# Kernel optimization log

Hardware: AMD Instinct MI355X
Metric: run time of the kernel (lower is better)

## Reference

```python
import jax, jax.numpy as jnp
import numpy as np

B, S, E = 2, 2048, 2048
H, KV, HD = 16, 4, 128  # num_heads, num_kv_heads, head_dim
G = H // KV             # query heads per kv head
ROPE_BASE = 10000.0


def rope_tables(dim, maxlen):
    freqs = 1.0 / ROPE_BASE ** (jnp.arange(0, dim, 2, dtype=jnp.float32) / dim)
    t = jnp.arange(maxlen, dtype=jnp.float32)
    f = jnp.outer(t, freqs)  # (maxlen, dim//2)
    return jnp.cos(f), jnp.sin(f)


def apply_rope(x, cos, sin):
    # x: (..., seq, heads, head_dim); interleaved-pair rotation
    s_len = x.shape[-3]
    c = cos[:s_len][:, None, :]
    s = sin[:s_len][:, None, :]
    x1 = x[..., ::2]
    x2 = x[..., 1::2]
    return jnp.stack([x1 * c - x2 * s, x1 * s + x2 * c], axis=-1).reshape(x.shape)


def setup_inputs() -> dict:
    key = jax.random.key(0)
    kx, kq, kk, kv, ko = jax.random.split(key, 5)
    x = jax.random.normal(kx, (B, S, E), dtype=jnp.float32)
    Wq = jax.random.normal(kq, (E, H * HD), dtype=jnp.float32) * 0.02
    Wk = jax.random.normal(kk, (E, KV * HD), dtype=jnp.float32) * 0.02
    Wv = jax.random.normal(kv, (E, KV * HD), dtype=jnp.float32) * 0.02
    Wo = jax.random.normal(ko, (H * HD, E), dtype=jnp.float32) * 0.02
    mask = jnp.tril(jnp.ones((S, S), dtype=bool))[None, None]  # causal (1,1,S,S)
    return {"x": x, "Wq": Wq, "Wk": Wk, "Wv": Wv, "Wo": Wo, "mask": mask}


def reference(x, Wq, Wk, Wv, Wo, mask):
    b, s, _ = x.shape
    cos, sin = rope_tables(HD, s)
    q = (x @ Wq).reshape(b, s, H, HD)
    k = (x @ Wk).reshape(b, s, KV, HD)
    v = (x @ Wv).reshape(b, s, KV, HD)
    q = apply_rope(q, cos, sin)
    k = apply_rope(k, cos, sin)
    if G > 1:
        k = jnp.repeat(k, G, axis=2)  # (b, s, H, HD)
        v = jnp.repeat(v, G, axis=2)
    q = jnp.transpose(q, (0, 2, 1, 3))  # (b, H, s, HD)
    k = jnp.transpose(k, (0, 2, 1, 3))
    v = jnp.transpose(v, (0, 2, 1, 3))
    scale = jnp.sqrt(jnp.float32(HD)).astype(q.dtype)
    scores = jnp.einsum("bhqd,bhkd->bhqk", q, k) / scale
    scores = jnp.where(mask, scores, jnp.finfo(scores.dtype).min)
    attn = jax.nn.softmax(scores, axis=-1)
    out = jnp.einsum("bhqk,bhkd->bhqd", attn, v)
    out = jnp.transpose(out, (0, 2, 1, 3)).reshape(b, s, H * HD)
    return out @ Wo
```

## Files before the change

kernel.cpp:

```cpp
#include <hip/hip_runtime.h>
#include <hip/hip_bf16.h>
#include <cstdint>

#define B_ 2
#define S_ 2048
#define E_ 2048
#define H_ 16
#define KV_ 4
#define HD_ 128
#define BS_ (B_*S_)
#define QKV_LD 3072
#define SM_SCALE 0.08838834764831845f
#define SC_LOG2E 0.1275424488538497f

typedef __attribute__((ext_vector_type(8))) __bf16 bf16x8;
typedef __attribute__((ext_vector_type(4))) float  floatx4;

__device__ __forceinline__ unsigned short f2bf(float f) {
  union { float f; unsigned u; } v; v.f = f;
  unsigned r = v.u + 0x7fffu + ((v.u >> 16) & 1u);
  return (unsigned short)(r >> 16);
}
__device__ __forceinline__ float bf2f(unsigned short u) {
  union { unsigned u; float f; } v; v.u = ((unsigned)u) << 16; return v.f;
}
__device__ __forceinline__ unsigned pack_bf16x2(float a, float b) {
  union { __hip_bfloat162 h; unsigned u; } v;
  v.h = __float22bfloat162_rn(make_float2(a, b));
  return v.u;
}

__device__ __forceinline__ void async_cp16(const void* g, void* l) {
  __builtin_amdgcn_global_load_lds(
      (const __attribute__((address_space(1))) void*)g,
      (__attribute__((address_space(3))) void*)l, 16, 0, 0);
}

__global__ __launch_bounds__(256)
void cvt_bf16(const float* __restrict__ src, unsigned short* __restrict__ dst,
              int n4) {
  int idx = blockIdx.x * 256 + threadIdx.x;
  if (idx >= n4) return;
  float4 v = *(const float4*)(src + (size_t)idx * 4);
  ushort4 o;
  o.x = f2bf(v.x); o.y = f2bf(v.y); o.z = f2bf(v.z); o.w = f2bf(v.w);
  *(ushort4*)(dst + (size_t)idx * 4) = o;
}

__global__ __launch_bounds__(256)
void cvt_bf16_t(const float* __restrict__ src, unsigned short* __restrict__ dst,
                int N, int dld, int noff) {
  __shared__ float tile[64 * 65];
  const int t = threadIdx.x;
  const int bk = blockIdx.y * 64, bn = blockIdx.x * 64;
  const int r = t >> 2, cg = t & 3;
#pragma unroll
  for (int i = 0; i < 4; ++i) {
    int c = cg * 16 + i * 4;
    float4 v = *(const float4*)(src + (size_t)(bk + r) * N + bn + c);
    tile[r * 65 + c] = v.x; tile[r * 65 + c + 1] = v.y;
    tile[r * 65 + c + 2] = v.z; tile[r * 65 + c + 3] = v.w;
  }
  __syncthreads();
  const int nl = t >> 2, kg = t & 3;
  union { unsigned short u[16]; uint4 q[2]; } o;
#pragma unroll
  for (int j = 0; j < 16; ++j)
    o.u[j] = f2bf(tile[(kg * 16 + j) * 65 + nl]);
  unsigned short* dp = dst + (size_t)(noff + bn + nl) * dld + bk + kg * 16;
  *(uint4*)(dp) = o.q[0];
  *(uint4*)(dp + 8) = o.q[1];
}

__global__ __launch_bounds__(256)
void rope_kernel(unsigned short* __restrict__ qkv) {
  const int PPR = 1280;
  int idx = blockIdx.x * 256 + threadIdx.x;
  if (idx >= BS_ * PPR) return;
  int row = idx / PPR, p = idx - row * PPR;
  int col = (p < 1024) ? (2 * p) : (2048 + 2 * (p - 1024));
  int d = p & 63;
  int s = row & (S_ - 1);
  float freq = expf(-(float)d * 0.14391156831212787f);
  float ang = (float)s * freq;
  float c = cosf(ang), sn = sinf(ang);
  unsigned short* ptr = qkv + (size_t)row * QKV_LD + col;
  float x1 = bf2f(ptr[0]), x2 = bf2f(ptr[1]);
  ptr[0] = f2bf(x1 * c - x2 * sn);
  ptr[1] = f2bf(x1 * sn + x2 * c);
}

__global__ __launch_bounds__(256)
void vtrans_kernel(const unsigned short* __restrict__ qkv,
                   unsigned short* __restrict__ vt) {
  __shared__ unsigned short tile[64 * 72];
  const int tid = threadIdx.x;
  const int s0 = blockIdx.x * 64;
  const int g = blockIdx.y >> 1;
  const int hh = (blockIdx.y & 1) * 64;
  const int b = g >> 2, kvh = g & 3;
#pragma unroll
  for (int i = 0; i < 2; ++i) {
    int chunk = tid + i * 256;
    int r = chunk >> 3, c = (chunk & 7) * 8;
    uint4 v = *(const uint4*)(qkv + (size_t)(b * S_ + s0 + r) * QKV_LD + 2560 + kvh * HD_ + hh + c);
    *(uint4*)(tile + r * 72 + c) = v;
  }
  __syncthreads();
#pragma unroll
  for (int i = 0; i < 2; ++i) {
    int chunk = tid + i * 256;
    int hdr = chunk >> 3, sc = (chunk & 7) * 8;
    union { unsigned short u[8]; uint4 v; } t;
#pragma unroll
    for (int j = 0; j < 8; ++j) t.u[j] = tile[(sc + j) * 72 + hdr];
    *(uint4*)(vt + (size_t)(g * HD_ + hh + hdr) * S_ + s0 + sc) = t.v;
  }
}

template<bool OUT_BF16>
__global__ __launch_bounds__(256, 2)
void gemm_tn(const unsigned short* __restrict__ A,
             const unsigned short* __restrict__ BT,
             void* __restrict__ C, int M, int N, int K) {
  __shared__ unsigned short Ash[128 * 32];
  __shared__ unsigned short Bsh[128 * 32];
  const int tid = threadIdx.x;
  const int l = tid & 63;
  const int l16 = l & 15, l4 = l >> 4;
  const int wave = tid >> 6;
  const int wm = (wave >> 1) * 64, wn = (wave & 1) * 64;
  const int bm = blockIdx.y * 128, bn = blockIdx.x * 128;

  const int srow = l >> 2;
  const int sg = (((l & 3) - (l >> 4)) & 3) * 8;

  floatx4 acc[4][4] = {};

  for (int kb = 0; kb < K; kb += 32) {
    __syncthreads();
#pragma unroll
    for (int i = 0; i < 2; ++i) {
      int cc = wave + i * 4;
      async_cp16(A + (size_t)(bm + 16 * cc + srow) * K + kb + sg, &Ash[cc * 512]);
      async_cp16(BT + (size_t)(bn + 16 * cc + srow) * K + kb + sg, &Bsh[cc * 512]);
    }
    __syncthreads();
    bf16x8 af[4], bf[4];
#pragma unroll
    for (int t = 0; t < 4; ++t) {
      int row = wm + t * 16 + l16;
      int s = (l4 + (l16 >> 2)) & 3;
      af[t] = *(const bf16x8*)(Ash + row * 32 + s * 8);
    }
#pragma unroll
    for (int t = 0; t < 4; ++t) {
      int row = wn + t * 16 + l16;
      int s = (l4 + (l16 >> 2)) & 3;
      bf[t] = *(const bf16x8*)(Bsh + row * 32 + s * 8);
    }
#pragma unroll
    for (int tm = 0; tm < 4; ++tm)
#pragma unroll
      for (int tn = 0; tn < 4; ++tn)
        acc[tm][tn] = __builtin_amdgcn_mfma_f32_16x16x32_bf16(af[tm], bf[tn], acc[tm][tn], 0, 0, 0);
  }
#pragma unroll
  for (int tm = 0; tm < 4; ++tm)
#pragma unroll
    for (int tn = 0; tn < 4; ++tn)
#pragma unroll
      for (int r = 0; r < 4; ++r) {
        int row = bm + wm + tm * 16 + l4 * 4 + r;
        int col = bn + wn + tn * 16 + l16;
        float v = acc[tm][tn][r];
        if (OUT_BF16) ((unsigned short*)C)[(size_t)row * N + col] = f2bf(v);
        else          ((float*)C)[(size_t)row * N + col] = v;
      }
}

__global__ __launch_bounds__(512, 2)
void gqa_attention(const unsigned short* __restrict__ qkv,
                   const unsigned short* __restrict__ vt,
                   unsigned short* __restrict__ out) {
  __shared__ unsigned short Ksh[2][2][32 * 128];
  __shared__ unsigned short Vsh[2][2][128 * 32];

  const int tid = threadIdx.x, l = tid & 63, wave = tid >> 6;
  const int l16 = l & 15, l4 = l >> 4;
  const int hw = wave & 3, seg = wave >> 2;
  const int g = blockIdx.x, b = g >> 2, kvh = g & 3;
  const int h = kvh * 4 + hw;
  const int y = blockIdx.y;

  const int k_subrow = l >> 4;
  const int v_subrow = l >> 2;
  const int gv = (((l & 3) - (l >> 4)) & 3) * 8;

  const unsigned short* kp[2];
  const unsigned short* vp[2];
#pragma unroll
  for (int i = 0; i < 2; ++i) {
    int cc = hw + i * 4;
    int krow = 4 * cc + k_subrow;
    int gk = (((l & 15) - krow) & 15) * 8;
    kp[i] = qkv + (size_t)(b * S_ + krow) * QKV_LD + 2048 + kvh * HD_ + gk;
    vp[i] = vt + (size_t)(g * HD_ + 16 * cc + v_subrow) * S_ + gv;
  }

  for (int phase = 0; phase < 2; ++phase) {
    const int t = phase ? (63 - y) : y;
    const int qt = t * 32;
    const int nch = t + 1;
    const int c0 = nch >> 1;
    const int st = nch - c0;

    bf16x8 qfA[4], qfB[4];
    {
      const unsigned short* qpA = qkv + (size_t)(b * S_ + qt + l16) * QKV_LD + h * HD_;
      const unsigned short* qpB = qpA + (size_t)16 * QKV_LD;
#pragma unroll
      for (int c = 0; c < 4; ++c) {
        qfA[c] = *(const bf16x8*)(qpA + c * 32 + l4 * 8);
        qfB[c] = *(const bf16x8*)(qpB + c * 32 + l4 * 8);
      }
    }
    asm volatile("s_waitcnt vmcnt(0)" ::: "memory");
    asm volatile("s_barrier" ::: "memory");

    {
      const int ci = (seg == 0) ? 0 : c0;
      const int ko = ci * 32 * QKV_LD, vo = ci * 32;
#pragma unroll
      for (int i = 0; i < 2; ++i) {
        int cc = hw + i * 4;
        async_cp16(kp[i] + ko, &Ksh[seg][0][cc * 512]);
        async_cp16(vp[i] + vo, &Vsh[seg][0][cc * 512]);
      }
    }

    float lsumA = 0.f, lsumB = 0.f;
    floatx4 accA[8] = {}, accB[8] = {};

    for (int step = 0; step < st; ++step) {
      const int cur = step & 1;
      asm volatile("s_barrier" ::: "memory");
      {
        const int cn = step + 1;
        const int cnext = (seg == 0) ? ((cn < c0) ? cn : 0)
                                     : ((cn < st) ? (c0 + cn) : 0);
        const int ko = cnext * 32 * QKV_LD, vo = cnext * 32;
#pragma unroll
        for (int i = 0; i < 2; ++i) {
          int cc = hw + i * 4;
          async_cp16(kp[i] + ko, &Ksh[seg][cur ^ 1][cc * 512]);
          async_cp16(vp[i] + vo, &Vsh[seg][cur ^ 1][cc * 512]);
        }
      }
      asm volatile("s_waitcnt vmcnt(4)\n\ts_barrier" ::: "memory");

      const bool active = (seg == 1) || (step < c0);
      if (active) {
        const bool tri = (seg == 1) && (step == st - 1);

        floatx4 sA[2] = {}, sB[2] = {};
#pragma unroll
        for (int half = 0; half < 2; ++half) {
          const int krow = half * 16 + l16;
#pragma unroll
          for (int c = 0; c < 4; ++c) {
            const int s = (c * 4 + l4 + l16) & 15;
            bf16x8 kf = *(const bf16x8*)(&Ksh[seg][cur][krow * 128 + s * 8]);
            sA[half] = __builtin_amdgcn_mfma_f32_16x16x32_bf16(kf, qfA[c], sA[half], 0, 0, 0);
            sB[half] = __builtin_amdgcn_mfma_f32_16x16x32_bf16(kf, qfB[c], sB[half], 0, 0, 0);
          }
        }

        float pA[8], pB[8];
#pragma unroll
        for (int half = 0; half < 2; ++half)
#pragma unroll
          for (int r = 0; r < 4; ++r) {
            float vA = fminf(sA[half][r] * SC_LOG2E, 80.f);
            float vB = fminf(sB[half][r] * SC_LOG2E, 80.f);
            if (tri) {
              int kk = half * 16 + l4 * 4 + r;
              if (kk > l16) vA = -3e38f;
              if (half == 1 && (l4 * 4 + r) > l16) vB = -3e38f;
            }
            float eA = exp2f(vA), eB = exp2f(vB);
            pA[half * 4 + r] = eA; lsumA += eA;
            pB[half * 4 + r] = eB; lsumB += eB;
          }

        unsigned a0 = pack_bf16x2(pA[0], pA[1]);
        unsigned a1 = pack_bf16x2(pA[2], pA[3]);
        unsigned a2 = pack_bf16x2(pA[4], pA[5]);
        unsigned a3 = pack_bf16x2(pA[6], pA[7]);
        asm("v_permlane32_swap_b32 %0, %1" : "+v"(a0), "+v"(a2));
        asm("v_permlane16_swap_b32 %0, %1" : "+v"(a0), "+v"(a2));
        asm("v_permlane32_swap_b32 %0, %1" : "+v"(a1), "+v"(a3));
        asm("v_permlane16_swap_b32 %0, %1" : "+v"(a1), "+v"(a3));
        unsigned b0 = pack_bf16x2(pB[0], pB[1]);
        unsigned b1 = pack_bf16x2(pB[2], pB[3]);
        unsigned b2 = pack_bf16x2(pB[4], pB[5]);
        unsigned b3 = pack_bf16x2(pB[6], pB[7]);
        asm("v_permlane32_swap_b32 %0, %1" : "+v"(b0), "+v"(b2));
        asm("v_permlane16_swap_b32 %0, %1" : "+v"(b0), "+v"(b2));
        asm("v_permlane32_swap_b32 %0, %1" : "+v"(b1), "+v"(b3));
        asm("v_permlane16_swap_b32 %0, %1" : "+v"(b1), "+v"(b3));
        union { unsigned w[4]; bf16x8 v8; } punA, punB;
        punA.w[0] = a0; punA.w[1] = a1; punA.w[2] = a2; punA.w[3] = a3;
        punB.w[0] = b0; punB.w[1] = b1; punB.w[2] = b2; punB.w[3] = b3;
        const bf16x8 pfA = punA.v8;
        const bf16x8 pfB = punB.v8;

#pragma unroll
        for (int u = 0; u < 8; ++u) {
          const int row = u * 16 + l16;
          const int s = (l4 + (l16 >> 2)) & 3;
          bf16x8 vf = *(const bf16x8*)(&Vsh[seg][cur][row * 32 + s * 8]);
          accA[u] = __builtin_amdgcn_mfma_f32_16x16x32_bf16(vf, pfA, accA[u], 0, 0, 0);
          accB[u] = __builtin_amdgcn_mfma_f32_16x16x32_bf16(vf, pfB, accB[u], 0, 0, 0);
        }
      }
    }

    asm volatile("s_waitcnt vmcnt(0)" ::: "memory");
    __syncthreads();
    float* combA = (float*)(&Ksh[0][0][0]);
    float* combL = (float*)(&Vsh[0][0][0]);
    if (seg == 1) {
#pragma unroll
      for (int u = 0; u < 8; ++u)
        *(floatx4*)(combA + ((hw * 8 + u) * 64 + l) * 4) = accA[u];
      combL[(hw * 64 + l) * 2]     = lsumA;
      combL[(hw * 64 + l) * 2 + 1] = lsumB;
    }
    __syncthreads();
    if (seg == 0) {
#pragma unroll
      for (int u = 0; u < 8; ++u)
        accA[u] += *(const floatx4*)(combA + ((hw * 8 + u) * 64 + l) * 4);
      lsumA += combL[(hw * 64 + l) * 2];
      lsumB += combL[(hw * 64 + l) * 2 + 1];
    }
    __syncthreads();
    if (seg == 1) {
#pragma unroll
      for (int u = 0; u < 8; ++u)
        *(floatx4*)(combA + ((hw * 8 + u) * 64 + l) * 4) = accB[u];
    }
    __syncthreads();
    if (seg == 0) {
#pragma unroll
      for (int u = 0; u < 8; ++u)
        accB[u] += *(const floatx4*)(combA + ((hw * 8 + u) * 64 + l) * 4);

      lsumA += __shfl_xor(lsumA, 16, 64);
      lsumA += __shfl_xor(lsumA, 32, 64);
      lsumB += __shfl_xor(lsumB, 16, 64);
      lsumB += __shfl_xor(lsumB, 32, 64);
      float invA = 1.0f / lsumA;
      float invB = 1.0f / lsumB;
      unsigned short* opA = out + (size_t)(b * S_ + qt + l16) * 2048 + h * HD_;
      unsigned short* opB = opA + (size_t)16 * 2048;
#pragma unroll
      for (int u = 0; u < 8; ++u) {
        uint2 oA, oB;
        oA.x = pack_bf16x2(accA[u][0] * invA, accA[u][1] * invA);
        oA.y = pack_bf16x2(accA[u][2] * invA, accA[u][3] * invA);
        *(uint2*)(opA + u * 16 + l4 * 4) = oA;
        oB.x = pack_bf16x2(accB[u][0] * invB, accB[u][1] * invB);
        oB.y = pack_bf16x2(accB[u][2] * invB, accB[u][3] * invB);
        *(uint2*)(opB + u * 16 + l4 * 4) = oB;
      }
    }
  }
}

extern "C" void kernel_launch(void* const* d_in, const int* in_sizes, int n_in,
                              void* d_out, int out_size, void* d_ws, size_t ws_size,
                              hipStream_t stream) {
  const float* x  = (const float*)d_in[0];
  const float* Wq = (const float*)d_in[1];
  const float* Wk = (const float*)d_in[2];
  const float* Wv = (const float*)d_in[3];
  const float* Wo = (const float*)d_in[4];
  float* out = (float*)d_out;

  char* ws = (char*)d_ws;
  unsigned short* xb    = (unsigned short*)(ws);
  unsigned short* wqkvT = (unsigned short*)(ws + 16777216);
  unsigned short* woT   = (unsigned short*)(ws + 29360128);
  unsigned short* qkv   = (unsigned short*)(ws + 37748736);
  unsigned short* attn  = (unsigned short*)(ws + 62914560);
  unsigned short* vt    = (unsigned short*)(ws);

  cvt_bf16<<<(4096 * 2048 / 4 + 255) / 256, 256, 0, stream>>>(x, xb, 4096 * 2048 / 4);
  cvt_bf16_t<<<dim3(32, 32), 256, 0, stream>>>(Wq, wqkvT, 2048, 2048, 0);
  cvt_bf16_t<<<dim3(8, 32),  256, 0, stream>>>(Wk, wqkvT, 512,  2048, 2048);
  cvt_bf16_t<<<dim3(8, 32),  256, 0, stream>>>(Wv, wqkvT, 512,  2048, 2560);
  cvt_bf16_t<<<dim3(32, 32), 256, 0, stream>>>(Wo, woT,  2048, 2048, 0);

  gemm_tn<true><<<dim3(24, 32), 256, 0, stream>>>(xb, wqkvT, qkv, 4096, 3072, 2048);
  rope_kernel<<<(4096 * 1280 + 255) / 256, 256, 0, stream>>>(qkv);
  vtrans_kernel<<<dim3(32, 16), 256, 0, stream>>>(qkv, vt);
  gqa_attention<<<dim3(8, 32), 512, 0, stream>>>(qkv, vt, attn);
  gemm_tn<false><<<dim3(16, 32), 256, 0, stream>>>(attn, woT, out, 4096, 2048, 2048);
}
```

Baseline: 338.0 us.

## Replace GEMM with 256x256 8-wave double-buffered pipelined kernel

Replaces the 128x128 single-buffer GEMM with a 256x256-tile, 512-thread kernel. It uses double-buffered LDS with K=64 steps, interleaves async loads with four MFMA quadrant phases, raises wave priority around MFMAs, and remaps workgroup IDs across 8 groups. The aim is to hide global load latency, halve the barrier count per unit of work and raise operand reuse in the QKV and output projections. It uses much more LDS (128KB per block) and more registers, and the grids become small (192 and 128 blocks), which may underfill the CUs.

```diff
diff --git a/kernel.cpp b/kernel.cpp
--- a/kernel.cpp
+++ b/kernel.cpp
@@ -119,64 +119,167 @@
 }
 
 template<bool OUT_BF16>
-__global__ __launch_bounds__(256, 2)
-void gemm_tn(const unsigned short* __restrict__ A,
-             const unsigned short* __restrict__ BT,
-             void* __restrict__ C, int M, int N, int K) {
-  __shared__ unsigned short Ash[128 * 32];
-  __shared__ unsigned short Bsh[128 * 32];
-  const int tid = threadIdx.x;
-  const int l = tid & 63;
+__global__ __launch_bounds__(512, 2)
+void gemm8(const unsigned short* __restrict__ A,
+           const unsigned short* __restrict__ BT,
+           void* __restrict__ C, int M, int N, int K) {
+  __shared__ unsigned short Ash[2][256 * 64];
+  __shared__ unsigned short Bsh[2][256 * 64];
+  const int tid = threadIdx.x, l = tid & 63, w = tid >> 6;
   const int l16 = l & 15, l4 = l >> 4;
-  const int wave = tid >> 6;
-  const int wm = (wave >> 1) * 64, wn = (wave & 1) * 64;
-  const int bm = blockIdx.y * 128, bn = blockIdx.x * 128;
-
-  const int srow = l >> 2;
-  const int sg = (((l & 3) - (l >> 4)) & 3) * 8;
-
-  floatx4 acc[4][4] = {};
-
-  for (int kb = 0; kb < K; kb += 32) {
-    __syncthreads();
-#pragma unroll
-    for (int i = 0; i < 2; ++i) {
-      int cc = wave + i * 4;
-      async_cp16(A + (size_t)(bm + 16 * cc + srow) * K + kb + sg, &Ash[cc * 512]);
-      async_cp16(BT + (size_t)(bn + 16 * cc + srow) * K + kb + sg, &Bsh[cc * 512]);
-    }
-    __syncthreads();
-    bf16x8 af[4], bf[4];
-#pragma unroll
-    for (int t = 0; t < 4; ++t) {
-      int row = wm + t * 16 + l16;
-      int s = (l4 + (l16 >> 2)) & 3;
-      af[t] = *(const bf16x8*)(Ash + row * 32 + s * 8);
-    }
-#pragma unroll
-    for (int t = 0; t < 4; ++t) {
-      int row = wn + t * 16 + l16;
-      int s = (l4 + (l16 >> 2)) & 3;
-      bf[t] = *(const bf16x8*)(Bsh + row * 32 + s * 8);
-    }
-#pragma unroll
-    for (int tm = 0; tm < 4; ++tm)
-#pragma unroll
-      for (int tn = 0; tn < 4; ++tn)
-        acc[tm][tn] = __builtin_amdgcn_mfma_f32_16x16x32_bf16(af[tm], bf[tn], acc[tm][tn], 0, 0, 0);
-  }
-#pragma unroll
-  for (int tm = 0; tm < 4; ++tm)
-#pragma unroll
-    for (int tn = 0; tn < 4; ++tn)
-#pragma unroll
-      for (int r = 0; r < 4; ++r) {
-        int row = bm + wm + tm * 16 + l4 * 4 + r;
-        int col = bn + wn + tn * 16 + l16;
-        float v = acc[tm][tn][r];
-        if (OUT_BF16) ((unsigned short*)C)[(size_t)row * N + col] = f2bf(v);
-        else          ((float*)C)[(size_t)row * N + col] = v;
-      }
+  const int w2 = w >> 2, w3 = w & 3;
+
+  const int ntn = (int)gridDim.x;
+  const int nwg = (int)(gridDim.x * gridDim.y);
+  const int orig = (int)blockIdx.y * ntn + (int)blockIdx.x;
+  const int cpx = nwg >> 3;
+  const int swz = (orig & 7) * cpx + (orig >> 3);
+  const int bm = (swz / ntn) * 256, bn = (swz % ntn) * 256;
+
+  const int srow = tid >> 3;
+  const int sgrp = ((tid & 7) - (tid >> 3)) & 7;
+  const unsigned short* Asrc = A  + (size_t)(bm + srow) * K + sgrp * 8;
+  const unsigned short* Bsrc = BT + (size_t)(bn + srow) * K + sgrp * 8;
+  const int ldst = w * 512;
+
+#define STAGE_A8(buf, H, kb) do { \
+    async_cp16(Asrc + (size_t)((H) * 128) * K + (kb),      &Ash[buf][(H) * 8192 + ldst]); \
+    async_cp16(Asrc + (size_t)((H) * 128 + 64) * K + (kb), &Ash[buf][(H) * 8192 + 4096 + ldst]); \
+  } while (0)
+#define STAGE_B8(buf, H, kb) do { \
+    async_cp16(Bsrc + (size_t)((H) * 128) * K + (kb),      &Bsh[buf][(H) * 8192 + ldst]); \
+    async_cp16(Bsrc + (size_t)((H) * 128 + 64) * K + (kb), &Bsh[buf][(H) * 8192 + 4096 + ldst]); \
+  } while (0)
+#define BAR8() __builtin_amdgcn_s_barrier()
+#define VMCNT4() asm volatile("s_waitcnt vmcnt(4)" ::: "memory")
+
+  const int s0 = ((l4 + l16) & 7) * 8;
+  const int s1 = ((l4 + l16 + 4) & 7) * 8;
+  const int arb = w2 * 64 + l16;
+  const int brb = w3 * 32 + l16;
+
+  const int nkt = K >> 6;
+
+  STAGE_B8(0, 0, 0);
+  STAGE_A8(0, 1, 0);
+  STAGE_A8(0, 0, 0);
+  STAGE_B8(0, 1, 0);
+  {
+    const int kb1 = (nkt > 1) ? 64 : 0;
+    STAGE_B8(1, 0, kb1);
+    STAGE_A8(1, 1, kb1);
+  }
+  VMCNT4(); BAR8();
+
+  floatx4 acc[2][4][2][2] = {};
+
+  for (int kt = 0; kt < nkt; ++kt) {
+    const int cur = kt & 1;
+    const int kb1 = ((kt + 1 < nkt) ? kt + 1 : nkt - 1) << 6;
+    const int kb2 = ((kt + 2 < nkt) ? kt + 2 : nkt - 1) << 6;
+    bf16x8 a[4][2], b0[2][2], b1[2][2];
+
+#pragma unroll
+    for (int m = 0; m < 4; ++m) {
+      const int rA = 128 + arb + m * 16;
+      a[m][0] = *(const bf16x8*)(&Ash[cur][rA * 64 + s0]);
+      a[m][1] = *(const bf16x8*)(&Ash[cur][rA * 64 + s1]);
+    }
+#pragma unroll
+    for (int n = 0; n < 2; ++n) {
+      const int rB = brb + n * 16;
+      b0[n][0] = *(const bf16x8*)(&Bsh[cur][rB * 64 + s0]);
+      b0[n][1] = *(const bf16x8*)(&Bsh[cur][rB * 64 + s1]);
+    }
+    STAGE_A8(cur ^ 1, 0, kb1);
+    BAR8();
+    __builtin_amdgcn_s_setprio(1);
+#pragma unroll
+    for (int m = 0; m < 4; ++m)
+#pragma unroll
+      for (int n = 0; n < 2; ++n) {
+        acc[1][m][0][n] = __builtin_amdgcn_mfma_f32_16x16x32_bf16(a[m][0], b0[n][0], acc[1][m][0][n], 0, 0, 0);
+        acc[1][m][0][n] = __builtin_amdgcn_mfma_f32_16x16x32_bf16(a[m][1], b0[n][1], acc[1][m][0][n], 0, 0, 0);
+      }
+    __builtin_amdgcn_s_setprio(0);
+    BAR8();
+
+#pragma unroll
+    for (int n = 0; n < 2; ++n) {
+      const int rB = 128 + brb + n * 16;
+      b1[n][0] = *(const bf16x8*)(&Bsh[cur][rB * 64 + s0]);
+      b1[n][1] = *(const bf16x8*)(&Bsh[cur][rB * 64 + s1]);
+    }
+    STAGE_B8(cur ^ 1, 1, kb1);
+    BAR8();
+    __builtin_amdgcn_s_setprio(1);
+#pragma unroll
+    for (int m = 0; m < 4; ++m)
+#pragma unroll
+      for (int n = 0; n < 2; ++n) {
+        acc[1][m][1][n] = __builtin_amdgcn_mfma_f32_16x16x32_bf16(a[m][0], b1[n][0], acc[1][m][1][n], 0, 0, 0);
+        acc[1][m][1][n] = __builtin_amdgcn_mfma_f32_16x16x32_bf16(a[m][1], b1[n][1], acc[1][m][1][n], 0, 0, 0);
+      }
+    __builtin_amdgcn_s_setprio(0);
+    BAR8();
+
+#pragma unroll
+    for (int m = 0; m < 4; ++m) {
+      const int rA = arb + m * 16;
+      a[m][0] = *(const bf16x8*)(&Ash[cur][rA * 64 + s0]);
+      a[m][1] = *(const bf16x8*)(&Ash[cur][rA * 64 + s1]);
+    }
+    STAGE_B8(cur, 0, kb2);
+    BAR8();
+    __builtin_amdgcn_s_setprio(1);
+#pragma unroll
+    for (int m = 0; m < 4; ++m)
+#pragma unroll
+      for (int n = 0; n < 2; ++n) {
+        acc[0][m][1][n] = __builtin_amdgcn_mfma_f32_16x16x32_bf16(a[m][0], b1[n][0], acc[0][m][1][n], 0, 0, 0);
+        acc[0][m][1][n] = __builtin_amdgcn_mfma_f32_16x16x32_bf16(a[m][1], b1[n][1], acc[0][m][1][n], 0, 0, 0);
+      }
+    __builtin_amdgcn_s_setprio(0);
+    BAR8();
+
+    STAGE_A8(cur, 1, kb2);
+    BAR8();
+    __builtin_amdgcn_s_setprio(1);
+#pragma unroll
+    for (int m = 0; m < 4; ++m)
+#pragma unroll
+      for (int n = 0; n < 2; ++n) {
+        acc[0][m][0][n] = __builtin_amdgcn_mfma_f32_16x16x32_bf16(a[m][0], b0[n][0], acc[0][m][0][n], 0, 0, 0);
+        acc[0][m][0][n] = __builtin_amdgcn_mfma_f32_16x16x32_bf16(a[m][1], b0[n][1], acc[0][m][0][n], 0, 0, 0);
+      }
+    __builtin_amdgcn_s_setprio(0);
+    VMCNT4();
+    BAR8();
+  }
+
+  asm volatile("s_waitcnt vmcnt(0)" ::: "memory");
+
+#pragma unroll
+  for (int mh = 0; mh < 2; ++mh)
+#pragma unroll
+    for (int m = 0; m < 4; ++m)
+#pragma unroll
+      for (int nh = 0; nh < 2; ++nh)
+#pragma unroll
+        for (int n = 0; n < 2; ++n) {
+          const int row0 = bm + mh * 128 + w2 * 64 + m * 16 + l4 * 4;
+          const int col  = bn + nh * 128 + w3 * 32 + n * 16 + l16;
+#pragma unroll
+          for (int rr = 0; rr < 4; ++rr) {
+            float v = acc[mh][m][nh][n][rr];
+            if (OUT_BF16) ((unsigned short*)C)[(size_t)(row0 + rr) * N + col] = f2bf(v);
+            else          ((float*)C)[(size_t)(row0 + rr) * N + col] = v;
+          }
+        }
+#undef STAGE_A8
+#undef STAGE_B8
+#undef BAR8
+#undef VMCNT4
 }
 
 __global__ __launch_bounds__(512, 2)
@@ -403,9 +506,9 @@
   cvt_bf16_t<<<dim3(8, 32),  256, 0, stream>>>(Wv, wqkvT, 512,  2048, 2560);
   cvt_bf16_t<<<dim3(32, 32), 256, 0, stream>>>(Wo, woT,  2048, 2048, 0);
 
-  gemm_tn<true><<<dim3(24, 32), 256, 0, stream>>>(xb, wqkvT, qkv, 4096, 3072, 2048);
+  gemm8<true><<<dim3(12, 16), 512, 0, stream>>>(xb, wqkvT, qkv, 4096, 3072, 2048);
   rope_kernel<<<(4096 * 1280 + 255) / 256, 256, 0, stream>>>(qkv);
   vtrans_kernel<<<dim3(32, 16), 256, 0, stream>>>(qkv, vt);
   gqa_attention<<<dim3(8, 32), 512, 0, stream>>>(qkv, vt, attn);
-  gemm_tn<false><<<dim3(16, 32), 256, 0, stream>>>(attn, woT, out, 4096, 2048, 2048);
-}
+  gemm8<false><<<dim3(8, 16), 512, 0, stream>>>(attn, woT, out, 4096, 2048, 2048);
+}
```

Measured after the change: 359.1 us. +6.2%, slower.

## Double-buffer GEMM LDS loads and fuse RoPE into QKV GEMM epilogue

Applied to the files above, without the earlier changes.

Restructures the GEMM main loop to double-buffer the A/B shared-memory tiles, issuing the async copies for the next k-tile before computing on the current one, and uses vmcnt waits with raw barriers. It also raises wave priority around the MFMA block. RoPE is now applied in the QKV GEMM epilogue through lane shuffles between adjacent columns, which removes the separate rope kernel launch and its read-modify-write pass over Q/K. The costs are twice the LDS per block, which may reduce occupancy, and per-element sin/cos in the epilogue. The final iteration also issues a redundant prefetch from offset 0.

```diff
diff --git a/kernel.cpp b/kernel.cpp
--- a/kernel.cpp
+++ b/kernel.cpp
@@ -73,24 +73,6 @@
 }
 
 __global__ __launch_bounds__(256)
-void rope_kernel(unsigned short* __restrict__ qkv) {
-  const int PPR = 1280;
-  int idx = blockIdx.x * 256 + threadIdx.x;
-  if (idx >= BS_ * PPR) return;
-  int row = idx / PPR, p = idx - row * PPR;
-  int col = (p < 1024) ? (2 * p) : (2048 + 2 * (p - 1024));
-  int d = p & 63;
-  int s = row & (S_ - 1);
-  float freq = expf(-(float)d * 0.14391156831212787f);
-  float ang = (float)s * freq;
-  float c = cosf(ang), sn = sinf(ang);
-  unsigned short* ptr = qkv + (size_t)row * QKV_LD + col;
-  float x1 = bf2f(ptr[0]), x2 = bf2f(ptr[1]);
-  ptr[0] = f2bf(x1 * c - x2 * sn);
-  ptr[1] = f2bf(x1 * sn + x2 * c);
-}
-
-__global__ __launch_bounds__(256)
 void vtrans_kernel(const unsigned short* __restrict__ qkv,
                    unsigned short* __restrict__ vt) {
   __shared__ unsigned short tile[64 * 72];
@@ -118,13 +100,13 @@
   }
 }
 
-template<bool OUT_BF16>
+template<bool OUT_BF16, bool ROPE>
 __global__ __launch_bounds__(256, 2)
 void gemm_tn(const unsigned short* __restrict__ A,
              const unsigned short* __restrict__ BT,
              void* __restrict__ C, int M, int N, int K) {
-  __shared__ unsigned short Ash[128 * 32];
-  __shared__ unsigned short Bsh[128 * 32];
+  __shared__ unsigned short Ash[2][128 * 32];
+  __shared__ unsigned short Bsh[2][128 * 32];
   const int tid = threadIdx.x;
   const int l = tid & 63;
   const int l16 = l & 15, l4 = l >> 4;
@@ -135,48 +117,90 @@
   const int srow = l >> 2;
   const int sg = (((l & 3) - (l >> 4)) & 3) * 8;
 
+  const unsigned short* ap[2];
+  const unsigned short* bp[2];
+#pragma unroll
+  for (int i = 0; i < 2; ++i) {
+    int cc = wave + i * 4;
+    ap[i] = A  + (size_t)(bm + 16 * cc + srow) * K + sg;
+    bp[i] = BT + (size_t)(bn + 16 * cc + srow) * K + sg;
+  }
+
+  const int nkt = K >> 5;
+
+#pragma unroll
+  for (int i = 0; i < 2; ++i) {
+    int cc = wave + i * 4;
+    async_cp16(ap[i], &Ash[0][cc * 512]);
+    async_cp16(bp[i], &Bsh[0][cc * 512]);
+  }
+
   floatx4 acc[4][4] = {};
 
-  for (int kb = 0; kb < K; kb += 32) {
-    __syncthreads();
-#pragma unroll
-    for (int i = 0; i < 2; ++i) {
-      int cc = wave + i * 4;
-      async_cp16(A + (size_t)(bm + 16 * cc + srow) * K + kb + sg, &Ash[cc * 512]);
-      async_cp16(BT + (size_t)(bn + 16 * cc + srow) * K + kb + sg, &Bsh[cc * 512]);
-    }
-    __syncthreads();
+  for (int it = 0; it < nkt; ++it) {
+    const int cur = it & 1;
+    asm volatile("s_barrier" ::: "memory");
+    {
+      const int kb2 = (it + 1 < nkt) ? (it + 1) * 32 : 0;
+#pragma unroll
+      for (int i = 0; i < 2; ++i) {
+        int cc = wave + i * 4;
+        async_cp16(ap[i] + kb2, &Ash[cur ^ 1][cc * 512]);
+        async_cp16(bp[i] + kb2, &Bsh[cur ^ 1][cc * 512]);
+      }
+    }
+    asm volatile("s_waitcnt vmcnt(4)\n\ts_barrier" ::: "memory");
+
     bf16x8 af[4], bf[4];
 #pragma unroll
     for (int t = 0; t < 4; ++t) {
       int row = wm + t * 16 + l16;
       int s = (l4 + (l16 >> 2)) & 3;
-      af[t] = *(const bf16x8*)(Ash + row * 32 + s * 8);
+      af[t] = *(const bf16x8*)(&Ash[cur][row * 32 + s * 8]);
     }
 #pragma unroll
     for (int t = 0; t < 4; ++t) {
       int row = wn + t * 16 + l16;
       int s = (l4 + (l16 >> 2)) & 3;
-      bf[t] = *(const bf16x8*)(Bsh + row * 32 + s * 8);
-    }
+      bf[t] = *(const bf16x8*)(&Bsh[cur][row * 32 + s * 8]);
+    }
+    __builtin_amdgcn_s_setprio(1);
 #pragma unroll
     for (int tm = 0; tm < 4; ++tm)
 #pragma unroll
       for (int tn = 0; tn < 4; ++tn)
         acc[tm][tn] = __builtin_amdgcn_mfma_f32_16x16x32_bf16(af[tm], bf[tn], acc[tm][tn], 0, 0, 0);
-  }
+    __builtin_amdgcn_s_setprio(0);
+  }
+
+  asm volatile("s_waitcnt vmcnt(0)" ::: "memory");
+
 #pragma unroll
   for (int tm = 0; tm < 4; ++tm)
 #pragma unroll
-    for (int tn = 0; tn < 4; ++tn)
+    for (int tn = 0; tn < 4; ++tn) {
+      const int row0 = bm + wm + tm * 16 + l4 * 4;
+      const int col  = bn + wn + tn * 16 + l16;
+      if (ROPE && col < 2560) {
+        const int d = (col & 127) >> 1;
+        const float freq = expf(-(float)d * 0.14391156831212787f);
+        const float sgn = (l & 1) ? 1.f : -1.f;
+#pragma unroll
+        for (int r = 0; r < 4; ++r) {
+          float own = acc[tm][tn][r];
+          float part = __shfl_xor(own, 1, 64);
+          float ang = (float)((row0 + r) & (S_ - 1)) * freq;
+          float cth = cosf(ang), sth = sinf(ang);
+          acc[tm][tn][r] = own * cth + part * sth * sgn;
+        }
+      }
 #pragma unroll
       for (int r = 0; r < 4; ++r) {
-        int row = bm + wm + tm * 16 + l4 * 4 + r;
-        int col = bn + wn + tn * 16 + l16;
         float v = acc[tm][tn][r];
-        if (OUT_BF16) ((unsigned short*)C)[(size_t)row * N + col] = f2bf(v);
-        else          ((float*)C)[(size_t)row * N + col] = v;
-      }
+        if (OUT_BF16) ((unsigned short*)C)[(size_t)(row0 + r) * N + col] = f2bf(v);
+        else          ((float*)C)[(size_t)(row0 + r) * N + col] = v;
+      }
+    }
 }
 
 __global__ __launch_bounds__(512, 2)
@@ -403,9 +427,8 @@
   cvt_bf16_t<<<dim3(8, 32),  256, 0, stream>>>(Wv, wqkvT, 512,  2048, 2560);
   cvt_bf16_t<<<dim3(32, 32), 256, 0, stream>>>(Wo, woT,  2048, 2048, 0);
 
-  gemm_tn<true><<<dim3(24, 32), 256, 0, stream>>>(xb, wqkvT, qkv, 4096, 3072, 2048);
-  rope_kernel<<<(4096 * 1280 + 255) / 256, 256, 0, stream>>>(qkv);
+  gemm_tn<true, true><<<dim3(24, 32), 256, 0, stream>>>(xb, wqkvT, qkv, 4096, 3072, 2048);
   vtrans_kernel<<<dim3(32, 16), 256, 0, stream>>>(qkv, vt);
   gqa_attention<<<dim3(8, 32), 512, 0, stream>>>(qkv, vt, attn);
-  gemm_tn<false><<<dim3(16, 32), 256, 0, stream>>>(attn, woT, out, 4096, 2048, 2048);
-}
+  gemm_tn<false, false><<<dim3(16, 32), 256, 0, stream>>>(attn, woT, out, 4096, 2048, 2048);
+}
```

Measured after the change: 362.5 us. 7.2% more time.
